# Optimization experiments

Hardware: AMD Instinct MI355X
Metric: run time of the kernel (lower is better)

## Reference

```python
import jax, jax.numpy as jnp
import numpy as np

B, S, D_IN, D_OUT, R, E = 4, 2048, 2048, 2048, 16, 8
SCALING = 16.0 / 16.0  # lora_alpha / r


def setup_inputs() -> dict:
    key = jax.random.key(0)
    ks = jax.random.split(key, 5)
    x = jax.random.normal(ks[0], (B, S, D_IN), dtype=jnp.float32)
    W = jax.random.normal(ks[1], (D_OUT, D_IN), dtype=jnp.float32) * (1.0 / np.sqrt(D_IN))
    b = jax.random.normal(ks[2], (D_OUT,), dtype=jnp.float32) * 0.01
    lora_A = jax.random.normal(ks[3], (E, R, D_IN), dtype=jnp.float32) * (1.0 / np.sqrt(D_IN))
    lora_B = jax.random.normal(ks[4], (E, D_OUT, R), dtype=jnp.float32) * 0.01
    expert_mask = jnp.ones((E,), dtype=bool)
    return {"x": x, "W": W, "b": b, "lora_A": lora_A, "lora_B": lora_B, "expert_mask": expert_mask}


def reference(x, W, b, lora_A, lora_B, expert_mask):
    # Base linear: [B,S,D_in] @ [D_in,D_out]
    result = jnp.einsum('bsd,od->bso', x, W) + b
    # Masked sum over experts of B_e(A_e(x)) * scaling.
    # Collapse the per-expert sum: effective_A = sum over selected experts done via
    # masked contraction; since delta = sum_e m_e * (x A_e^T) B_e^T, fold mask into A.
    mA = lora_A * expert_mask.astype(x.dtype)[:, None, None]  # [E,R,D_in]
    z = jnp.einsum('bsd,erd->bser', x, mA)                     # [B,S,E,R]
    delta = jnp.einsum('bser,eor->bso', z, lora_B)             # [B,S,D_out]
    return result + delta * SCALING
```

## Files before the change

### kernel.cpp

```cpp
#include <hip/hip_runtime.h>
#include <stdint.h>

typedef __bf16 bf16x8 __attribute__((ext_vector_type(8)));
typedef float  f32x4  __attribute__((ext_vector_type(4)));
typedef float  float4v __attribute__((ext_vector_type(4)));
typedef short  short8 __attribute__((ext_vector_type(8)));
typedef short  short4v __attribute__((ext_vector_type(4)));

static constexpr int Mtot = 8192;
static constexpr int Ntot = 2048;
static constexpr int Ktot = 2048;
static constexpr int NE = 8, NR = 16;
static constexpr int ERTOT = NE * NR;
static constexpr float SCALING = 16.0f / 16.0f;

__device__ __forceinline__ ushort f2bf(float f) {
  union { float f; uint32_t u; } v; v.f = f;
  uint32_t r = (v.u + 0x7FFFu + ((v.u >> 16) & 1u)) >> 16;
  return (ushort)r;
}

__device__ __forceinline__ void lds16(const void* g, void* l) {
  __builtin_amdgcn_global_load_lds(
      (const __attribute__((address_space(1))) void*)g,
      (__attribute__((address_space(3))) void*)l, 16, 0, 0);
}

__global__ __launch_bounds__(256) void k_prep(const float* __restrict__ x,
                                              ushort* __restrict__ xb,
                                              const float* __restrict__ W,
                                              const float* __restrict__ lA,
                                              const float* __restrict__ lB,
                                              const int* __restrict__ mask,
                                              ushort* __restrict__ Wb) {
  __shared__ float bv[16][ERTOT + 1];
  int tid = threadIdx.x;
  if (blockIdx.x < 8192) {
    size_t i = ((size_t)blockIdx.x * 256 + tid) * 8;
    float4v a = *reinterpret_cast<const float4v*>(x + i);
    float4v c = *reinterpret_cast<const float4v*>(x + i + 4);
    short8 o;
    o[0] = (short)f2bf(a[0]); o[1] = (short)f2bf(a[1]);
    o[2] = (short)f2bf(a[2]); o[3] = (short)f2bf(a[3]);
    o[4] = (short)f2bf(c[0]); o[5] = (short)f2bf(c[1]);
    o[6] = (short)f2bf(c[2]); o[7] = (short)f2bf(c[3]);
    *reinterpret_cast<short8*>(xb + i) = o;
  } else {
    int bid = blockIdx.x - 8192;
    int o0 = (bid & 127) * 16;
    int d0 = (bid >> 7) * 64;
    for (int t = tid; t < 16 * ERTOT; t += 256) {
      int r = t >> 7, i = t & 127;
      int e = i >> 4, rr = i & 15;
      float m = (mask[e] != 0) ? SCALING : 0.0f;
      bv[r][i] = lB[((size_t)e * Ntot + (o0 + r)) * NR + rr] * m;
    }
    __syncthreads();
    int tx = tid & 15, ty = tid >> 4;
    int d = d0 + tx * 4;
    int o = o0 + ty;
    float4v acc = *reinterpret_cast<const float4v*>(W + (size_t)o * Ktot + d);
    #pragma unroll 4
    for (int i = 0; i < ERTOT; ++i) {
      float bw = bv[ty][i];
      float4v av = *reinterpret_cast<const float4v*>(lA + (size_t)i * Ktot + d);
      acc[0] += bw * av[0]; acc[1] += bw * av[1];
      acc[2] += bw * av[2]; acc[3] += bw * av[3];
    }
    short4v s;
    s[0] = (short)f2bf(acc[0]); s[1] = (short)f2bf(acc[1]);
    s[2] = (short)f2bf(acc[2]); s[3] = (short)f2bf(acc[3]);
    *reinterpret_cast<short4v*>(Wb + (size_t)o * Ktot + d) = s;
  }
}

__global__ __launch_bounds__(512, 2) void k_gemm256(const ushort* __restrict__ Xb,
                                                    const ushort* __restrict__ Wb,
                                                    const float* __restrict__ bias,
                                                    float* __restrict__ out) {
  constexpr int BK = 32;
  constexpr int NT = Ktot / BK;
  constexpr int NTN = Ntot / 256;
  __shared__ __align__(128) char smem[4 * 32768];

  int nwg = gridDim.x;
  int orig = blockIdx.x;
  int wg = (orig & 7) * (nwg >> 3) + (orig >> 3);
  int mBase = (wg / NTN) * 256;
  int nBase = (wg % NTN) * 256;

  int tid = threadIdx.x;
  int w = tid >> 6, l = tid & 63;
  int wr = w >> 2, wc = w & 3;

  int rowOff = tid >> 2;
  int cbS = ((tid & 3) * 16) ^ (((tid >> 3) & 3) << 4);
  const char* xbB = (const char*)Xb;
  const char* wbB = (const char*)Wb;
  const char* src[4];
  src[0] = xbB + (size_t)(mBase +       rowOff) * (Ktot * 2) + cbS;
  src[1] = xbB + (size_t)(mBase + 128 + rowOff) * (Ktot * 2) + cbS;
  src[2] = wbB + (size_t)(nBase +       rowOff) * (Ktot * 2) + cbS;
  src[3] = wbB + (size_t)(nBase + 128 + rowOff) * (Ktot * 2) + cbS;
  int waveB = w * 1024;

  auto stage = [&](int bufn, int which, size_t kb) {
    lds16(src[which] + kb, smem + bufn * 32768 + which * 8192 + waveB);
  };

  int fr = l & 15;
  int fkb = (l >> 4) * 16;
  int kx = fkb ^ (((fr >> 1) & 3) << 4);
  int aRd = (wr * 128 + fr) * 64 + kx;
  int bRd = 16384 + (wc * 64 + fr) * 64 + kx;

  f32x4 acc[8][4];
  #pragma unroll
  for (int i = 0; i < 8; ++i)
    #pragma unroll
    for (int j = 0; j < 4; ++j) acc[i][j] = f32x4{0.f, 0.f, 0.f, 0.f};

  bf16x8 aF[4], bF[4];

  #pragma unroll
  for (int q = 0; q < 4; ++q) stage(0, q, 0);
  #pragma unroll
  for (int q = 0; q < 4; ++q) stage(1, q, 64);
  __syncthreads();

  for (int t = 0; t < NT; ++t) {
    const char* buf = smem + (t & 3) * 32768;
    const bool pref = (t + 2 < NT);
    const int bn = (t + 2) & 3;
    const size_t kb = (size_t)(t + 2) * 64;

    #pragma unroll
    for (int mi = 0; mi < 4; ++mi)
      aF[mi] = *reinterpret_cast<const bf16x8*>(buf + aRd + mi * 1024);
    #pragma unroll
    for (int nj = 0; nj < 4; ++nj)
      bF[nj] = *reinterpret_cast<const bf16x8*>(buf + bRd + nj * 1024);
    if (pref) { stage(bn, 0, kb); stage(bn, 1, kb); }
    __builtin_amdgcn_s_barrier();
    __builtin_amdgcn_s_setprio(1);
    #pragma unroll
    for (int mi = 0; mi < 4; ++mi)
      #pragma unroll
      for (int nj = 0; nj < 4; ++nj)
        acc[mi][nj] = __builtin_amdgcn_mfma_f32_16x16x32_bf16(aF[mi], bF[nj], acc[mi][nj], 0, 0, 0);
    __builtin_amdgcn_s_setprio(0);
    __builtin_amdgcn_s_barrier();

    #pragma unroll
    for (int mi = 0; mi < 4; ++mi)
      aF[mi] = *reinterpret_cast<const bf16x8*>(buf + aRd + (4 + mi) * 1024);
    if (pref) { stage(bn, 2, kb); stage(bn, 3, kb); }
    __builtin_amdgcn_s_barrier();
    __builtin_amdgcn_s_setprio(1);
    #pragma unroll
    for (int mi = 0; mi < 4; ++mi)
      #pragma unroll
      for (int nj = 0; nj < 4; ++nj)
        acc[4 + mi][nj] = __builtin_amdgcn_mfma_f32_16x16x32_bf16(aF[mi], bF[nj], acc[4 + mi][nj], 0, 0, 0);
    __builtin_amdgcn_s_setprio(0);

    if (t + 2 < NT)      asm volatile("s_waitcnt vmcnt(4)" ::: "memory");
    else if (t + 1 < NT) asm volatile("s_waitcnt vmcnt(0)" ::: "memory");
    __builtin_amdgcn_s_barrier();
  }

  int rr = (l >> 4) * 4;
  #pragma unroll
  for (int nj = 0; nj < 4; ++nj) {
    int col = nBase + wc * 64 + nj * 16 + fr;
    float bb = bias[col];
    #pragma unroll
    for (int mi = 0; mi < 8; ++mi) {
      int row0 = mBase + wr * 128 + mi * 16 + rr;
      #pragma unroll
      for (int r = 0; r < 4; ++r)
        out[(size_t)(row0 + r) * Ntot + col] = acc[mi][nj][r] + bb;
    }
  }
}

extern "C" void kernel_launch(void* const* d_in, const int* in_sizes, int n_in,
                              void* d_out, int out_size, void* d_ws, size_t ws_size,
                              hipStream_t stream) {
  const float* x    = (const float*)d_in[0];
  const float* W    = (const float*)d_in[1];
  const float* bias = (const float*)d_in[2];
  const float* lA   = (const float*)d_in[3];
  const float* lB   = (const float*)d_in[4];
  const int*   mask = (const int*)d_in[5];
  float* out = (float*)d_out;

  ushort* xb = (ushort*)d_ws;
  ushort* wb = xb + (size_t)Mtot * Ktot;

  k_prep<<<8192 + 4096, 256, 0, stream>>>(x, xb, W, lA, lB, mask, wb);
  k_gemm256<<<(Mtot / 256) * (Ntot / 256), 512, 0, stream>>>(xb, wb, bias, out);
}
```

Baseline: 258.4 us.

## Compute folded LoRA weight with MFMA kernel instead of scalar FMA prep

The effective weight W + B·A (rank 128) was built with scalar FP32 FMAs inside the prep kernel. It is now computed in a separate MFMA kernel: the prep kernel transposes and converts lora_A and lora_B to bf16, and a new kernel does the 2048x2048x128 product with swizzled LDS tiles and adds W before the bf16 store. This removes the scalar FMA work and the repeated lora_A reads from prep. In exchange it adds a kernel launch and lowers the precision of the LoRA term to bf16 inputs. The x conversion also changes its access pattern to 4-wide loads split across two halves.

```diff
diff --git a/kernel.cpp b/kernel.cpp
--- a/kernel.cpp
+++ b/kernel.cpp
@@ -11,7 +11,7 @@
 static constexpr int Ntot = 2048;
 static constexpr int Ktot = 2048;
 static constexpr int NE = 8, NR = 16;
-static constexpr int ERTOT = NE * NR;
+static constexpr int R2 = NE * NR;
 static constexpr float SCALING = 16.0f / 16.0f;
 
 __device__ __forceinline__ ushort f2bf(float f) {
@@ -28,49 +28,117 @@
 
 __global__ __launch_bounds__(256) void k_prep(const float* __restrict__ x,
                                               ushort* __restrict__ xb,
-                                              const float* __restrict__ W,
                                               const float* __restrict__ lA,
                                               const float* __restrict__ lB,
                                               const int* __restrict__ mask,
-                                              ushort* __restrict__ Wb) {
-  __shared__ float bv[16][ERTOT + 1];
+                                              ushort* __restrict__ Abt,
+                                              ushort* __restrict__ Bst) {
   int tid = threadIdx.x;
   if (blockIdx.x < 8192) {
-    size_t i = ((size_t)blockIdx.x * 256 + tid) * 8;
-    float4v a = *reinterpret_cast<const float4v*>(x + i);
-    float4v c = *reinterpret_cast<const float4v*>(x + i + 4);
-    short8 o;
-    o[0] = (short)f2bf(a[0]); o[1] = (short)f2bf(a[1]);
-    o[2] = (short)f2bf(a[2]); o[3] = (short)f2bf(a[3]);
-    o[4] = (short)f2bf(c[0]); o[5] = (short)f2bf(c[1]);
-    o[6] = (short)f2bf(c[2]); o[7] = (short)f2bf(c[3]);
-    *reinterpret_cast<short8*>(xb + i) = o;
+    size_t base = (size_t)blockIdx.x * 2048;
+    int t4 = tid * 4;
+    float4v a = *reinterpret_cast<const float4v*>(x + base + t4);
+    float4v c = *reinterpret_cast<const float4v*>(x + base + 1024 + t4);
+    short4v s0, s1;
+    s0[0] = (short)f2bf(a[0]); s0[1] = (short)f2bf(a[1]);
+    s0[2] = (short)f2bf(a[2]); s0[3] = (short)f2bf(a[3]);
+    s1[0] = (short)f2bf(c[0]); s1[1] = (short)f2bf(c[1]);
+    s1[2] = (short)f2bf(c[2]); s1[3] = (short)f2bf(c[3]);
+    *reinterpret_cast<short4v*>(xb + base + t4) = s0;
+    *reinterpret_cast<short4v*>(xb + base + 1024 + t4) = s1;
+  } else if (blockIdx.x < 8200) {
+    int d = (blockIdx.x - 8192) * 256 + tid;
+    short8 buf[16];
+    #pragma unroll 8
+    for (int i = 0; i < R2; ++i)
+      ((short*)buf)[i] = (short)f2bf(lA[(size_t)i * Ktot + d]);
+    #pragma unroll
+    for (int q = 0; q < 16; ++q)
+      *reinterpret_cast<short8*>(Abt + (size_t)d * R2 + q * 8) = buf[q];
   } else {
-    int bid = blockIdx.x - 8192;
-    int o0 = (bid & 127) * 16;
-    int d0 = (bid >> 7) * 64;
-    for (int t = tid; t < 16 * ERTOT; t += 256) {
-      int r = t >> 7, i = t & 127;
-      int e = i >> 4, rr = i & 15;
+    int o = (blockIdx.x - 8200) * 256 + tid;
+    short8 buf[16];
+    #pragma unroll
+    for (int e = 0; e < NE; ++e) {
       float m = (mask[e] != 0) ? SCALING : 0.0f;
-      bv[r][i] = lB[((size_t)e * Ntot + (o0 + r)) * NR + rr] * m;
+      #pragma unroll
+      for (int rg = 0; rg < 4; ++rg) {
+        float4v v = *reinterpret_cast<const float4v*>(lB + ((size_t)e * Ntot + o) * NR + rg * 4);
+        ((short*)buf)[e * 16 + rg * 4 + 0] = (short)f2bf(v[0] * m);
+        ((short*)buf)[e * 16 + rg * 4 + 1] = (short)f2bf(v[1] * m);
+        ((short*)buf)[e * 16 + rg * 4 + 2] = (short)f2bf(v[2] * m);
+        ((short*)buf)[e * 16 + rg * 4 + 3] = (short)f2bf(v[3] * m);
+      }
     }
-    __syncthreads();
-    int tx = tid & 15, ty = tid >> 4;
-    int d = d0 + tx * 4;
-    int o = o0 + ty;
-    float4v acc = *reinterpret_cast<const float4v*>(W + (size_t)o * Ktot + d);
-    #pragma unroll 4
-    for (int i = 0; i < ERTOT; ++i) {
-      float bw = bv[ty][i];
-      float4v av = *reinterpret_cast<const float4v*>(lA + (size_t)i * Ktot + d);
-      acc[0] += bw * av[0]; acc[1] += bw * av[1];
-      acc[2] += bw * av[2]; acc[3] += bw * av[3];
+    #pragma unroll
+    for (int q = 0; q < 16; ++q)
+      *reinterpret_cast<short8*>(Bst + (size_t)o * R2 + q * 8) = buf[q];
+  }
+}
+
+__global__ __launch_bounds__(256) void k_weff_mfma(const ushort* __restrict__ Bst,
+                                                   const ushort* __restrict__ Abt,
+                                                   const float* __restrict__ W,
+                                                   ushort* __restrict__ Wb) {
+  __shared__ __align__(128) char sA[32768];
+  __shared__ __align__(128) char sB[32768];
+  int bid = blockIdx.x;
+  int o0 = (bid >> 4) * 128;
+  int d0 = (bid & 15) * 128;
+  int tid = threadIdx.x, w = tid >> 6, l = tid & 63;
+
+  int srow = w * 32 + (l >> 4);
+  int scolb = (l & 15) * 16;
+  #pragma unroll
+  for (int j = 0; j < 8; ++j) {
+    int row = srow + j * 4;
+    int colb = scolb ^ ((row & 7) << 4);
+    lds16((const char*)Bst + (size_t)(o0 + row) * 256 + colb, sA + w * 8192 + j * 1024);
+    lds16((const char*)Abt + (size_t)(d0 + row) * 256 + colb, sB + w * 8192 + j * 1024);
+  }
+  __syncthreads();
+
+  int wr = w >> 1, wc = w & 1;
+  int fr = l & 15;
+  int fk16 = (l >> 4) * 16;
+  int xm = (fr & 7) << 4;
+
+  f32x4 acc[4][4];
+  #pragma unroll
+  for (int i = 0; i < 4; ++i)
+    #pragma unroll
+    for (int j = 0; j < 4; ++j) acc[i][j] = f32x4{0.f, 0.f, 0.f, 0.f};
+
+  #pragma unroll
+  for (int ks = 0; ks < 4; ++ks) {
+    int kx = (ks * 64 + fk16) ^ xm;
+    bf16x8 aF[4], bF[4];
+    #pragma unroll
+    for (int mi = 0; mi < 4; ++mi)
+      aF[mi] = *reinterpret_cast<const bf16x8*>(sA + (wr * 64 + mi * 16 + fr) * 256 + kx);
+    #pragma unroll
+    for (int nj = 0; nj < 4; ++nj)
+      bF[nj] = *reinterpret_cast<const bf16x8*>(sB + (wc * 64 + nj * 16 + fr) * 256 + kx);
+    #pragma unroll
+    for (int mi = 0; mi < 4; ++mi)
+      #pragma unroll
+      for (int nj = 0; nj < 4; ++nj)
+        acc[mi][nj] = __builtin_amdgcn_mfma_f32_16x16x32_bf16(aF[mi], bF[nj], acc[mi][nj], 0, 0, 0);
+  }
+
+  int rr4 = (l >> 4) * 4;
+  #pragma unroll
+  for (int nj = 0; nj < 4; ++nj) {
+    int col = d0 + wc * 64 + nj * 16 + fr;
+    #pragma unroll
+    for (int mi = 0; mi < 4; ++mi) {
+      int row0 = o0 + wr * 64 + mi * 16 + rr4;
+      #pragma unroll
+      for (int r = 0; r < 4; ++r) {
+        float v = acc[mi][nj][r] + W[(size_t)(row0 + r) * Ktot + col];
+        Wb[(size_t)(row0 + r) * Ktot + col] = f2bf(v);
+      }
     }
-    short4v s;
-    s[0] = (short)f2bf(acc[0]); s[1] = (short)f2bf(acc[1]);
-    s[2] = (short)f2bf(acc[2]); s[3] = (short)f2bf(acc[3]);
-    *reinterpret_cast<short4v*>(Wb + (size_t)o * Ktot + d) = s;
   }
 }
 
@@ -195,9 +263,12 @@
   const int*   mask = (const int*)d_in[5];
   float* out = (float*)d_out;
 
-  ushort* xb = (ushort*)d_ws;
-  ushort* wb = xb + (size_t)Mtot * Ktot;
-
-  k_prep<<<8192 + 4096, 256, 0, stream>>>(x, xb, W, lA, lB, mask, wb);
+  ushort* xb  = (ushort*)d_ws;
+  ushort* wb  = xb + (size_t)Mtot * Ktot;
+  ushort* abt = wb + (size_t)Ntot * Ktot;
+  ushort* bst = abt + (size_t)Ktot * R2;
+
+  k_prep<<<8192 + 8 + 8, 256, 0, stream>>>(x, xb, lA, lB, mask, abt, bst);
+  k_weff_mfma<<<(Ntot / 128) * (Ktot / 128), 256, 0, stream>>>(bst, abt, W, wb);
   k_gemm256<<<(Mtot / 256) * (Ntot / 256), 512, 0, stream>>>(xb, wb, bias, out);
 }
```

After: 213.3 us. -17.4%, faster.
